# Performance work log

Hardware: AMD Instinct MI355X
Metric: run time of the kernel (lower is better)

## Reference

```python
import jax, jax.numpy as jnp
import numpy as np

B, M, N, I, O, NM = 32, 128, 128, 64, 64, 16


def setup_inputs() -> dict:
    key = jax.random.key(0)
    ks = jax.random.split(key, 10)
    def p(k, shape, s=0.02):
        return jax.random.normal(k, shape, jnp.float32) * s
    g = 1.0 / (I * O)  # xavier_normal_ gain=1/(in*out) -> tiny weights
    return {
        "x": jax.random.normal(ks[0], (B, M, N, I), jnp.float32),
        "w_spec0": p(ks[1], (2, I, O, NM, 2), g),
        "w_spec1": p(ks[2], (2, I, O, NM, 2), g),
        "w_lin": p(ks[3], (I, O)), "b_lin": jnp.zeros((O,), jnp.float32),
        "w_b1": p(ks[4], (O, 2 * O)), "b_b1": jnp.zeros((2 * O,), jnp.float32),
        "w_b2": p(ks[5], (2 * O, O)), "b_b2": jnp.zeros((O,), jnp.float32),
        "w_f1": p(ks[6], (O, 2 * O)), "b_f1": jnp.zeros((2 * O,), jnp.float32),
        "w_f2": p(ks[7], (2 * O, O)), "b_f2": jnp.zeros((O,), jnp.float32),
    }


def _complex_matmul_2d(a, w):
    # a: complex [B, I, x, y]; w: real [2, I, O, NM, 2] (factorized x-weight, y-weight)
    w0 = w[0][..., 0] + 1j * w[0][..., 1]  # [I, O, NM] complex, applied along x
    w1 = w[1][..., 0] + 1j * w[1][..., 1]  # [I, O, NM] complex, applied along y
    c = jnp.einsum('iox,bixy->boxy', w0, a)
    return jnp.einsum('bixy,ioy->boxy', c, w1)


def reference(x, w_spec0, w_spec1, w_lin, b_lin, w_b1, b_b1, w_b2, b_b2,
              w_f1, b_f1, w_f2, b_f2):
    Bv, Mv, Nv, Iv = x.shape
    nm = w_spec0.shape[3]
    Ov = w_spec0.shape[2]
    # residual branch (conv_norm=False -> Identity norm)
    res = x @ w_lin + b_lin  # [B, M, N, O]
    # spectral branch
    xt = jnp.transpose(x, (0, 3, 1, 2))  # [B, I, M, N]
    x_ft = jnp.fft.rfft2(xt, s=(Mv, Nv), norm='ortho')  # [B, I, M, N//2+1] complex64
    out_ft = jnp.zeros((Bv, Ov, Nv, Mv // 2 + 1), dtype=x_ft.dtype)  # M==N in this config
    out_ft = out_ft.at[:, :, :nm, :nm].set(_complex_matmul_2d(x_ft[:, :, :nm, :nm], w_spec0))
    out_ft = out_ft.at[:, :, -nm:, :nm].set(_complex_matmul_2d(x_ft[:, :, -nm:, :nm], w_spec1))
    y = jnp.fft.irfft2(out_ft, s=(Nv, Mv), norm='ortho')  # [B, O, N, M]
    y = jnp.transpose(y, (0, 2, 3, 1))  # [B, M, N, O]
    y = jax.nn.relu(y + res)
    bcast = jax.nn.relu(y @ w_b1 + b_b1) @ w_b2 + b_b2
    fcast = jax.nn.relu(y @ w_f1 + b_f1) @ w_f2 + b_f2
    return (bcast, fcast)
```

## Files before the change

kernel.cpp:

```cpp
#include <hip/hip_runtime.h>
#include <hip/hip_bf16.h>

#define TWO_PI 6.28318530717958647692f

typedef __attribute__((ext_vector_type(8))) short bf16x8;
typedef __attribute__((ext_vector_type(4))) float f32x4;

__device__ __forceinline__ unsigned short f2bf(float v) {
    __hip_bfloat16 h = __float2bfloat16(v);
    return *(unsigned short*)&h;
}

__device__ __forceinline__ bf16x8 cvt8(float4 a, float4 b) {
    bf16x8 r;
    r[0] = (short)f2bf(a.x); r[1] = (short)f2bf(a.y);
    r[2] = (short)f2bf(a.z); r[3] = (short)f2bf(a.w);
    r[4] = (short)f2bf(b.x); r[5] = (short)f2bf(b.y);
    r[6] = (short)f2bf(b.z); r[7] = (short)f2bf(b.w);
    return r;
}


__global__ __launch_bounds__(256) void k0_prep(const float* __restrict__ ws0,
                                               const float* __restrict__ ws1,
                                               float2* __restrict__ w0t,
                                               float2* __restrict__ w1t)
{
    int tgt = blockIdx.x * 256 + threadIdx.x;
    if (tgt < 131072) {
        int p = tgt >> 12;
        int rem = tgt & 4095;
        int i = rem >> 6, j = rem & 63;
        const float* s = (p < 16) ? ws0 : ws1;
        int px = p & 15;
        int base = ((i * 64 + j) * 16 + px) * 2;
        w0t[tgt] = make_float2(s[base], s[base + 1]);
    } else {
        int u = tgt - 131072;
        int h = u >> 16;
        int kv = (u >> 12) & 15;
        int j = (u >> 6) & 63;
        int o = u & 63;
        const float* s = (h ? ws1 : ws0) + 131072;
        int base = ((j * 64 + o) * 16 + kv) * 2;
        w1t[u] = make_float2(s[base], s[base + 1]);
    }
}

__global__ __launch_bounds__(256) void k0b_prep(const float* __restrict__ wb1,
                                                const float* __restrict__ wf1,
                                                const float* __restrict__ wb2,
                                                const float* __restrict__ wf2,
                                                const float* __restrict__ wl,
                                                unsigned short* __restrict__ w1bt,
                                                unsigned short* __restrict__ w2bt,
                                                unsigned short* __restrict__ wlt_pre,
                                                unsigned short* __restrict__ ctb_pre,
                                                unsigned short* __restrict__ wdft,
                                                unsigned short* __restrict__ e2k2,
                                                unsigned short* __restrict__ e2k4)
{
    int tgt = blockIdx.x * 256 + threadIdx.x;
    if (tgt < 16384) {
        int head = tgt >> 13;
        int o = (tgt >> 6) & 127;
        int i = tgt & 63;
        const float* src = head ? wf1 : wb1;
        int dst = head * 8192 + o * 64 + (((i >> 3) ^ (o & 7)) << 3) + (i & 7);
        w1bt[dst] = f2bf(src[i * 128 + o]);
    } else if (tgt < 32768) {
        int u = tgt - 16384;
        int head = u >> 13;
        int o = (u >> 7) & 63;
        int c = u & 127;
        const float* src = head ? wf2 : wb2;
        int dst = head * 8192 + o * 128 + (((c >> 3) ^ (o & 7)) << 3) + (c & 7);
        w2bt[dst] = f2bf(src[c * 64 + o]);
    } else if (tgt < 36864) {
        int u = tgt - 32768;
        int o = u >> 6, i = u & 63;
        int chunk = (i >> 3) ^ (o & 7);
        wlt_pre[o * 64 + chunk * 8 + (i & 7)] = f2bf(wl[i * 64 + o]);
    } else if (tgt < 40960) {
        int u = tgt - 36864;
        int v = u >> 5, k = u & 31;
        float val;
        if (k < 16) {
            val = (k == 0) ? (1.0f / 128.0f)
                           : (2.0f / 128.0f) * cosf(TWO_PI * k * v * (1.0f / 128.0f));
        } else {
            int q = k - 16;
            val = (q == 0) ? 0.f
                           : -(2.0f / 128.0f) * sinf(TWO_PI * q * v * (1.0f / 128.0f));
        }
        int chunk = (k >> 3) ^ ((v >> 1) & 3);
        ctb_pre[v * 32 + chunk * 8 + (k & 7)] = f2bf(val);
    } else if (tgt < 45312) {
        int u = tgt - 40960;
        int c = u / 2176;
        int rem = u - c * 2176;
        int kv = rem / 136, n = rem - (rem / 136) * 136;
        float val = 0.f;
        if (n < 128) {
            int idx = (kv * n) & 127;
            float th = (float)idx * (TWO_PI / 128.0f);
            val = c ? -sinf(th) : cosf(th);
        }
        wdft[u] = f2bf(val);
    } else if (tgt < 61696) {
        int u = tgt - 45312;
        int plane = u >> 13;
        int rem = u & 8191;
        int p = rem >> 8;
        int k = rem & 255;
        int km = (p < 16) ? p : (96 + p);
        int m = (k < 128) ? k : (k - 128);
        float th = (float)((km * m) & 127) * (TWO_PI / 128.0f);
        float c = cosf(th), s = sinf(th);
        float val = plane ? ((k < 128) ? -s : c) : ((k < 128) ? c : s);
        val *= (1.0f / 128.0f);
        int ch = k >> 3;
        int dst = plane * 8192 + p * 256 + (((ch & 24) | ((ch ^ p) & 7)) << 3) + (k & 7);
        e2k2[dst] = f2bf(val);
    } else {
        int u = tgt - 61696;
        int plane = u >> 13;
        int rem = u & 8191;
        int uu = rem >> 6;
        int k = rem & 63;
        int p = (k < 32) ? k : (k - 32);
        int km = (p < 16) ? p : (96 + p);
        float th = (float)((km * uu) & 127) * (TWO_PI / 128.0f);
        float c = cosf(th), s = sinf(th);
        float val = plane ? ((k < 32) ? s : c) : ((k < 32) ? c : -s);
        int ch = k >> 3;
        int dst = plane * 8192 + uu * 64 + (((ch ^ (uu & 7)) & 7) << 3) + (k & 7);
        e2k4[dst] = f2bf(val);
    }
}

__global__ __launch_bounds__(256) void k1_dft_n(const float* __restrict__ x,
                                                const unsigned short* __restrict__ wdft,
                                                unsigned int* __restrict__ A)
{
    __shared__ __align__(16) unsigned short Xt[64 * 136];
    __shared__ __align__(16) unsigned short Wl[2 * 16 * 136];
    const int t = threadIdx.x;
    const int bm = blockIdx.x;
    {
        const uint4* wg = (const uint4*)wdft;
        uint4* wl = (uint4*)Wl;
        for (int k = t; k < 544; k += 256) wl[k] = wg[k];
    }
    {
        const float* xg = x + (size_t)bm * 8192;
        const int i = t & 63, q = t >> 6;
        #pragma unroll
        for (int pass = 0; pass < 8; ++pass) {
            int n0 = pass * 16 + q * 4;
            float v0 = xg[(n0 + 0) * 64 + i];
            float v1 = xg[(n0 + 1) * 64 + i];
            float v2 = xg[(n0 + 2) * 64 + i];
            float v3 = xg[(n0 + 3) * 64 + i];
            unsigned lo = (unsigned)f2bf(v0) | ((unsigned)f2bf(v1) << 16);
            unsigned hi = (unsigned)f2bf(v2) | ((unsigned)f2bf(v3) << 16);
            *(uint2*)&Xt[i * 136 + n0] = make_uint2(lo, hi);
        }
    }
    __syncthreads();
    const int lane = t & 63, wv = t >> 6;
    const int ar = lane & 15, kg = lane >> 4;
    f32x4 are = (f32x4){0.f, 0.f, 0.f, 0.f};
    f32x4 aim = (f32x4){0.f, 0.f, 0.f, 0.f};
    #pragma unroll
    for (int ks = 0; ks < 4; ++ks) {
        int off = ks * 32 + kg * 8;
        bf16x8 b   = *(const bf16x8*)&Xt[(wv * 16 + ar) * 136 + off];
        bf16x8 wre = *(const bf16x8*)&Wl[ar * 136 + off];
        bf16x8 wim = *(const bf16x8*)&Wl[(16 + ar) * 136 + off];
        are = __builtin_amdgcn_mfma_f32_16x16x32_bf16(wre, b, are, 0, 0, 0);
        aim = __builtin_amdgcn_mfma_f32_16x16x32_bf16(wim, b, aim, 0, 0, 0);
    }
    unsigned int* Ap = A + (size_t)bm * 1024;
    #pragma unroll
    for (int r = 0; r < 4; ++r) {
        int kv = kg * 4 + r;
        int i = wv * 16 + ar;
        Ap[kv * 64 + i] = (unsigned)f2bf(are[r]) | ((unsigned)f2bf(aim[r]) << 16);
    }
}

__global__ __launch_bounds__(256) void k2_dft_m(const unsigned int* __restrict__ A,
                                                const unsigned short* __restrict__ e2k2,
                                                float2* __restrict__ xft)
{
    __shared__ __align__(16) unsigned short El[16384];
    __shared__ __align__(16) unsigned short Sl[16384];
    const int t = threadIdx.x;
    const int b = blockIdx.x >> 4, kv = blockIdx.x & 15;
    {
        const uint4* eg = (const uint4*)e2k2;
        for (int k = t; k < 2048; k += 256) ((uint4*)El)[k] = eg[k];
    }
    for (int idx = t; idx < 4096; idx += 256) {
        int m2 = idx >> 6, i = idx & 63;
        int m = m2 << 1;
        unsigned a0 = A[((size_t)(b * 128 + m) * 16 + kv) * 64 + i];
        unsigned a1 = A[((size_t)(b * 128 + m + 1) * 16 + kv) * 64 + i];
        unsigned arp = (a0 & 0xffffu) | (a1 << 16);
        unsigned aip = (a0 >> 16) | (a1 & 0xffff0000u);
        int chr = m >> 3;
        *(unsigned*)&Sl[i * 256 + (((chr & 24) | ((chr ^ i) & 7)) << 3) + (m & 7)] = arp;
        int kk = 128 + m;
        int chi = kk >> 3;
        *(unsigned*)&Sl[i * 256 + (((chi & 24) | ((chi ^ i) & 7)) << 3) + (kk & 7)] = aip;
    }
    __syncthreads();
    const int lane = t & 63, wv = t >> 6;
    const int ar = lane & 15, kg = lane >> 4;
    const int pt = wv >> 1;
    const int it0 = (wv & 1) << 1;
    #pragma unroll
    for (int iti = 0; iti < 2; ++iti) {
        int it = it0 + iti;
        int prow = pt * 16 + ar;
        int irow = it * 16 + ar;
        f32x4 accre = (f32x4){0.f, 0.f, 0.f, 0.f};
        f32x4 accim = (f32x4){0.f, 0.f, 0.f, 0.f};
        #pragma unroll
        for (int ks = 0; ks < 8; ++ks) {
            int ch = ks * 4 + kg;
            int aoff = prow * 256 + (((ch & 24) | ((ch ^ prow) & 7)) << 3);
            int boff = irow * 256 + (((ch & 24) | ((ch ^ irow) & 7)) << 3);
            bf16x8 bfrag = *(const bf16x8*)&Sl[boff];
            bf16x8 fre = *(const bf16x8*)&El[aoff];
            bf16x8 fim = *(const bf16x8*)&El[8192 + aoff];
            accre = __builtin_amdgcn_mfma_f32_16x16x32_bf16(fre, bfrag, accre, 0, 0, 0);
            accim = __builtin_amdgcn_mfma_f32_16x16x32_bf16(fim, bfrag, accim, 0, 0, 0);
        }
        #pragma unroll
        for (int r = 0; r < 4; ++r) {
            int p = pt * 16 + kg * 4 + r;
            int i = it * 16 + ar;
            xft[((size_t)(b * 32 + p) * 16 + kv) * 64 + i] =
                make_float2(accre[r], accim[r]);
        }
    }
}

__global__ __launch_bounds__(256) void k3a_spec1(const float2* __restrict__ xft,
                                                 const float2* __restrict__ w0t,
                                                 float2* __restrict__ c1)
{
    __shared__ __align__(16) float2 xs[16][64];
    __shared__ __align__(16) float2 w0s[64][64];
    const int t = threadIdx.x;
    const int b = blockIdx.x >> 5, p = blockIdx.x & 31;
    const float2* xg = xft + (size_t)(b * 32 + p) * 1024;
    for (int k = t; k < 1024; k += 256) ((float2*)xs)[k] = xg[k];
    const float4* wg = (const float4*)(w0t + (size_t)p * 4096);
    for (int k = t; k < 2048; k += 256) ((float4*)w0s)[k] = wg[k];
    __syncthreads();
    const int j = t & 63;
    const int kv0 = (t >> 6) << 2;
    float2 acc[4];
    #pragma unroll
    for (int q = 0; q < 4; ++q) acc[q] = make_float2(0.f, 0.f);
    for (int i = 0; i < 64; ++i) {
        float2 w = w0s[i][j];
        #pragma unroll
        for (int q = 0; q < 4; ++q) {
            float2 a = xs[kv0 + q][i];
            acc[q].x += a.x * w.x - a.y * w.y;
            acc[q].y += a.x * w.y + a.y * w.x;
        }
    }
    #pragma unroll
    for (int q = 0; q < 4; ++q)
        c1[((size_t)(b * 32 + p) * 16 + kv0 + q) * 64 + j] = acc[q];
}

__global__ __launch_bounds__(256) void k3b_spec2(const float2* __restrict__ c1,
                                                 const float2* __restrict__ w1t,
                                                 float2* __restrict__ oft)
{
    __shared__ __align__(16) float2 cs[16][64];
    __shared__ __align__(16) float2 w1s[64][64];
    const int t = threadIdx.x;
    int id = blockIdx.x;
    const int h = id & 1; id >>= 1;
    const int kv = id & 15; const int b = id >> 4;
    for (int k = t; k < 1024; k += 256) {
        int pp = k >> 6, j = k & 63;
        cs[pp][j] = c1[((size_t)(b * 32 + h * 16 + pp) * 16 + kv) * 64 + j];
    }
    const float4* wg = (const float4*)(w1t + (size_t)(h * 16 + kv) * 4096);
    for (int k = t; k < 2048; k += 256) ((float4*)w1s)[k] = wg[k];
    __syncthreads();
    const int o = t & 63;
    const int pp0 = (t >> 6) << 2;
    float2 acc[4];
    #pragma unroll
    for (int q = 0; q < 4; ++q) acc[q] = make_float2(0.f, 0.f);
    for (int j = 0; j < 64; ++j) {
        float2 w = w1s[j][o];
        #pragma unroll
        for (int q = 0; q < 4; ++q) {
            float2 a = cs[pp0 + q][j];
            acc[q].x += a.x * w.x - a.y * w.y;
            acc[q].y += a.x * w.y + a.y * w.x;
        }
    }
    #pragma unroll
    for (int q = 0; q < 4; ++q)
        oft[((size_t)(b * 32 + h * 16 + pp0 + q) * 16 + kv) * 64 + o] = acc[q];
}

__global__ __launch_bounds__(256) void k4_idft_m(const float2* __restrict__ oft,
                                                 const unsigned short* __restrict__ e2k4,
                                                 unsigned int* __restrict__ T)
{
    __shared__ __align__(16) unsigned short El[16384];
    __shared__ __align__(16) unsigned short Sl[4096];
    const int t = threadIdx.x;
    const int b = blockIdx.x >> 4, q = blockIdx.x & 15;
    {
        const uint4* eg = (const uint4*)e2k4;
        for (int k = t; k < 2048; k += 256) ((uint4*)El)[k] = eg[k];
    }
    for (int idx = t; idx < 1024; idx += 256) {
        int p2 = idx >> 6, o = idx & 63;
        int p = p2 << 1;
        float2 v0 = oft[((size_t)(b * 32 + p) * 16 + q) * 64 + o];
        float2 v1 = oft[((size_t)(b * 32 + p + 1) * 16 + q) * 64 + o];
        unsigned rep = (unsigned)f2bf(v0.x) | ((unsigned)f2bf(v1.x) << 16);
        unsigned imp = (unsigned)f2bf(v0.y) | ((unsigned)f2bf(v1.y) << 16);
        int chr = p >> 3;
        *(unsigned*)&Sl[o * 64 + ((chr ^ (o & 7)) << 3) + (p & 7)] = rep;
        int kk = 32 + p;
        int chi = kk >> 3;
        *(unsigned*)&Sl[o * 64 + ((chi ^ (o & 7)) << 3) + (kk & 7)] = imp;
    }
    __syncthreads();
    const int lane = t & 63, wv = t >> 6;
    const int ar = lane & 15, kg = lane >> 4;
    unsigned int* Tp = T + ((size_t)b * 128) * 1024 + (size_t)q * 64;
    #pragma unroll
    for (int uti = 0; uti < 2; ++uti) {
        int ut = wv * 2 + uti;
        int urow = ut * 16 + ar;
        int aswz = urow & 7;
        #pragma unroll
        for (int ot = 0; ot < 4; ++ot) {
            int orow = ot * 16 + ar;
            f32x4 accre = (f32x4){0.f, 0.f, 0.f, 0.f};
            f32x4 accim = (f32x4){0.f, 0.f, 0.f, 0.f};
            #pragma unroll
            for (int ks = 0; ks < 2; ++ks) {
                int ch = ks * 4 + kg;
                int aoff = urow * 64 + ((ch ^ aswz) << 3);
                int boff = orow * 64 + ((ch ^ (orow & 7)) << 3);
                bf16x8 bfrag = *(const bf16x8*)&Sl[boff];
                bf16x8 fre = *(const bf16x8*)&El[aoff];
                bf16x8 fim = *(const bf16x8*)&El[8192 + aoff];
                accre = __builtin_amdgcn_mfma_f32_16x16x32_bf16(fre, bfrag, accre, 0, 0, 0);
                accim = __builtin_amdgcn_mfma_f32_16x16x32_bf16(fim, bfrag, accim, 0, 0, 0);
            }
            #pragma unroll
            for (int r = 0; r < 4; ++r) {
                int u = ut * 16 + kg * 4 + r;
                int o = ot * 16 + ar;
                Tp[(size_t)u * 1024 + o] =
                    (unsigned)f2bf(accre[r]) | ((unsigned)f2bf(accim[r]) << 16);
            }
        }
    }
}

__global__ __launch_bounds__(256) void k56_fused(
    const float* __restrict__ x, const unsigned int* __restrict__ Tg,
    const float* __restrict__ bl,
    const unsigned short* __restrict__ ctb_pre, const unsigned short* __restrict__ wlt_pre,
    const unsigned short* __restrict__ w1bt, const unsigned short* __restrict__ w2bt,
    const float* __restrict__ bb1, const float* __restrict__ bb2,
    const float* __restrict__ bf1, const float* __restrict__ bf2,
    float* __restrict__ out)
{
    __shared__ __align__(16) unsigned char U[32768];
    __shared__ __align__(16) unsigned short ys[2][8192];
    __shared__ __align__(16) unsigned short hs[8192];

    unsigned short* Ctb = (unsigned short*)U;
    unsigned short* wlt = (unsigned short*)(U + 8192);
    unsigned short* Tpk = (unsigned short*)(U + 16384);
    unsigned short* w1s = (unsigned short*)U;
    unsigned short* w2s = (unsigned short*)(U + 16384);

    const int t = threadIdx.x;
    const int bm0 = blockIdx.x << 1;
    const int lane = t & 63, wv = t >> 6;
    const int ar = lane & 15, kg = lane >> 4;
    const int R0 = wv * 32;

    float4 xr[2][2][4];
    #pragma unroll
    for (int g = 0; g < 2; ++g)
        #pragma unroll
        for (int rt = 0; rt < 2; ++rt) {
            const float* xp = x + (size_t)(bm0 + g) * 8192 + (R0 + rt * 16 + ar) * 64 + kg * 8;
            xr[g][rt][0] = *(const float4*)(xp);
            xr[g][rt][1] = *(const float4*)(xp + 4);
            xr[g][rt][2] = *(const float4*)(xp + 32);
            xr[g][rt][3] = *(const float4*)(xp + 36);
        }

    {
        const uint4* cg = (const uint4*)ctb_pre;
        for (int k = t; k < 512; k += 256) ((uint4*)Ctb)[k] = cg[k];
        const uint4* wg = (const uint4*)wlt_pre;
        for (int k = t; k < 512; k += 256) ((uint4*)wlt)[k] = wg[k];
        for (int idx = t; idx < 2048; idx += 256) {
            int g = idx >> 10, rem = idx & 1023;
            int q = rem >> 6, o = rem & 63;
            unsigned v = Tg[(size_t)(bm0 + g) * 1024 + rem];
            int f = (o >> 1) & 3;
            unsigned short* Tp = Tpk + g * 2048;
            Tp[o * 32 + (((q >> 3) ^ f) << 3) + (q & 7)] = (unsigned short)(v & 0xffffu);
            Tp[o * 32 + (((2 + (q >> 3)) ^ f) << 3) + (q & 7)] = (unsigned short)(v >> 16);
        }
    }
    __syncthreads();

    float biasl[4];
    #pragma unroll
    for (int ct = 0; ct < 4; ++ct) biasl[ct] = bl[ct * 16 + ar];

    #pragma unroll
    for (int g = 0; g < 2; ++g) {
        const unsigned short* Tp = Tpk + g * 2048;
        #pragma unroll
        for (int rt = 0; rt < 2; ++rt) {
            const int vrow = R0 + rt * 16 + ar;
            bf16x8 a0 = cvt8(xr[g][rt][0], xr[g][rt][1]);
            bf16x8 a1 = cvt8(xr[g][rt][2], xr[g][rt][3]);
            bf16x8 asp = *(const bf16x8*)&Ctb[vrow * 32 + ((kg ^ ((vrow >> 1) & 3)) << 3)];
            f32x4 acc[4];
            #pragma unroll
            for (int ct = 0; ct < 4; ++ct) acc[ct] = (f32x4){0.f, 0.f, 0.f, 0.f};
            #pragma unroll
            for (int ct = 0; ct < 4; ++ct) {
                int o = ct * 16 + ar;
                bf16x8 b0 = *(const bf16x8*)&wlt[o * 64 + ((kg ^ (o & 7)) << 3)];
                bf16x8 b1 = *(const bf16x8*)&wlt[o * 64 + (((4 + kg) ^ (o & 7)) << 3)];
                bf16x8 bsp = *(const bf16x8*)&Tp[o * 32 + ((kg ^ ((o >> 1) & 3)) << 3)];
                acc[ct] = __builtin_amdgcn_mfma_f32_16x16x32_bf16(a0, b0, acc[ct], 0, 0, 0);
                acc[ct] = __builtin_amdgcn_mfma_f32_16x16x32_bf16(a1, b1, acc[ct], 0, 0, 0);
                acc[ct] = __builtin_amdgcn_mfma_f32_16x16x32_bf16(asp, bsp, acc[ct], 0, 0, 0);
            }
            #pragma unroll
            for (int ct = 0; ct < 4; ++ct) {
                int col = ct * 16 + ar;
                #pragma unroll
                for (int r = 0; r < 4; ++r) {
                    int row = R0 + rt * 16 + kg * 4 + r;
                    float v = fmaxf(acc[ct][r] + biasl[ct], 0.f);
                    ys[g][row * 64 + (((col >> 3) ^ (row & 7)) << 3) + (col & 7)] = f2bf(v);
                }
            }
        }
    }
    __syncthreads();

    unsigned short* hw = hs + wv * 2048;
    for (int head = 0; head < 2; ++head) {
        {
            const uint4* g1 = (const uint4*)(w1bt + head * 8192);
            for (int k = t; k < 1024; k += 256) ((uint4*)w1s)[k] = g1[k];
            const uint4* g2 = (const uint4*)(w2bt + head * 8192);
            for (int k = t; k < 1024; k += 256) ((uint4*)w2s)[k] = g2[k];
        }
        const float* B1 = head ? bf1 : bb1;
        const float* B2 = head ? bf2 : bb2;
        float bias1[8], bias2[4];
        #pragma unroll
        for (int c = 0; c < 8; ++c) bias1[c] = B1[c * 16 + ar];
        #pragma unroll
        for (int c = 0; c < 4; ++c) bias2[c] = B2[c * 16 + ar];
        __syncthreads();

        #pragma unroll
        for (int g = 0; g < 2; ++g) {
            #pragma unroll
            for (int rt = 0; rt < 2; ++rt) {
                const int rowbase = R0 + rt * 16;
                const int yrow = rowbase + ar;
                bf16x8 ya0 = *(const bf16x8*)&ys[g][yrow * 64 + ((kg ^ (yrow & 7)) << 3)];
                bf16x8 ya1 = *(const bf16x8*)&ys[g][yrow * 64 + (((4 + kg) ^ (yrow & 7)) << 3)];
                f32x4 acc1[8];
                #pragma unroll
                for (int ct = 0; ct < 8; ++ct) acc1[ct] = (f32x4){0.f, 0.f, 0.f, 0.f};
                #pragma unroll
                for (int ct = 0; ct < 8; ++ct) {
                    int brow = ct * 16 + ar;
                    bf16x8 b0 = *(const bf16x8*)&w1s[brow * 64 + ((kg ^ (brow & 7)) << 3)];
                    bf16x8 b1 = *(const bf16x8*)&w1s[brow * 64 + (((4 + kg) ^ (brow & 7)) << 3)];
                    acc1[ct] = __builtin_amdgcn_mfma_f32_16x16x32_bf16(ya0, b0, acc1[ct], 0, 0, 0);
                    acc1[ct] = __builtin_amdgcn_mfma_f32_16x16x32_bf16(ya1, b1, acc1[ct], 0, 0, 0);
                }
                #pragma unroll
                for (int ct = 0; ct < 8; ++ct) {
                    #pragma unroll
                    for (int r = 0; r < 4; ++r) {
                        int row = kg * 4 + r;
                        int col = ct * 16 + ar;
                        float v = fmaxf(acc1[ct][r] + bias1[ct], 0.f);
                        hw[row * 128 + (((col >> 3) ^ (row & 7)) << 3) + (col & 7)] = f2bf(v);
                    }
                }
                f32x4 acc2[4];
                #pragma unroll
                for (int ct = 0; ct < 4; ++ct) acc2[ct] = (f32x4){0.f, 0.f, 0.f, 0.f};
                #pragma unroll
                for (int ks = 0; ks < 4; ++ks) {
                    bf16x8 a = *(const bf16x8*)&hw[ar * 128 + (((ks * 4 + kg) ^ (ar & 7)) << 3)];
                    #pragma unroll
                    for (int ct = 0; ct < 4; ++ct) {
                        int brow = ct * 16 + ar;
                        bf16x8 b = *(const bf16x8*)&w2s[brow * 128 + (((ks * 4 + kg) ^ (ar & 7)) << 3)];
                        acc2[ct] = __builtin_amdgcn_mfma_f32_16x16x32_bf16(a, b, acc2[ct], 0, 0, 0);
                    }
                }
                float* og = out + (size_t)head * 33554432u + (size_t)(bm0 + g) * 8192;
                #pragma unroll
                for (int ct = 0; ct < 4; ++ct) {
                    #pragma unroll
                    for (int r = 0; r < 4; ++r)
                        og[(size_t)(rowbase + kg * 4 + r) * 64 + ct * 16 + ar] =
                            acc2[ct][r] + bias2[ct];
                }
            }
        }
        if (head == 0) __syncthreads();
    }
}

extern "C" void kernel_launch(void* const* d_in, const int* in_sizes, int n_in,
                              void* d_out, int out_size, void* d_ws, size_t ws_size,
                              hipStream_t stream)
{
    (void)in_sizes; (void)n_in; (void)out_size; (void)ws_size;
    const float* x   = (const float*)d_in[0];
    const float* ws0 = (const float*)d_in[1];
    const float* ws1 = (const float*)d_in[2];
    const float* wl  = (const float*)d_in[3];
    const float* bl  = (const float*)d_in[4];
    const float* wb1 = (const float*)d_in[5];
    const float* bb1 = (const float*)d_in[6];
    const float* wb2 = (const float*)d_in[7];
    const float* bb2 = (const float*)d_in[8];
    const float* wf1 = (const float*)d_in[9];
    const float* bf1 = (const float*)d_in[10];
    const float* wf2 = (const float*)d_in[11];
    const float* bf2 = (const float*)d_in[12];
    float* out = (float*)d_out;

    float* ws = (float*)d_ws;
    float2* w0t = (float2*)ws;
    float2* w1t = (float2*)(ws + 262144);
    unsigned int* Tb  = (unsigned int*)(ws + 524288);
    unsigned int* Ab  = (unsigned int*)(ws + 8912896);
    float2* xft = (float2*)(ws + 17301504);
    float2* c1b = (float2*)(ws + 19398656);
    float2* oft = (float2*)(ws + 21495808);
    unsigned short* w1bt    = (unsigned short*)(ws + 23592960);
    unsigned short* w2bt    = (unsigned short*)(ws + 23601152);
    unsigned short* wlt_pre = (unsigned short*)(ws + 23609344);
    unsigned short* ctb_pre = (unsigned short*)(ws + 23611392);
    unsigned short* wdft    = (unsigned short*)(ws + 23613440);
    unsigned short* e2k2    = (unsigned short*)(ws + 23615616);
    unsigned short* e2k4    = (unsigned short*)(ws + 23623808);

    k0_prep    <<<1024, 256, 0, stream>>>(ws0, ws1, w0t, w1t);
    k0b_prep   <<<305,  256, 0, stream>>>(wb1, wf1, wb2, wf2, wl,
                                          w1bt, w2bt, wlt_pre, ctb_pre, wdft,
                                          e2k2, e2k4);
    k1_dft_n   <<<4096, 256, 0, stream>>>(x, wdft, Ab);
    k2_dft_m   <<<512,  256, 0, stream>>>(Ab, e2k2, xft);
    k3a_spec1  <<<1024, 256, 0, stream>>>(xft, w0t, c1b);
    k3b_spec2  <<<1024, 256, 0, stream>>>(c1b, w1t, oft);
    k4_idft_m  <<<512,  256, 0, stream>>>(oft, e2k4, Tb);
    k56_fused  <<<2048, 256, 0, stream>>>(x, Tb, bl, ctb_pre, wlt_pre,
                                          w1bt, w2bt, bb1, bb2, bf1, bf2, out);
}
```

Before: 218.2 us.

## Run spectral mode-mixing matmuls on bf16 MFMA with packed bf16 intermediates

Replaces the scalar fp32 complex multiply-accumulate loops in the two spectral weight kernels with bf16 MFMA instructions. Weights are pre-laid-out as real-block complex matrices ([re,-im; im,re]) in swizzled bf16 tiles. The intermediates between the DFT, spectral and inverse-DFT stages are stored as packed bf16 re/im pairs instead of float2, halving that memory traffic. This trades precision for throughput, and the weight prep kernel now launches more threads to write the expanded layout.

```diff
diff --git a/kernel.cpp b/kernel.cpp
--- a/kernel.cpp
+++ b/kernel.cpp
@@ -20,31 +20,36 @@
     return r;
 }
 
+#define SWZ128(row, ch) ((((ch) & 8) | (((ch) ^ ((row) & 7)) & 7)) << 3)
+
 
 __global__ __launch_bounds__(256) void k0_prep(const float* __restrict__ ws0,
                                                const float* __restrict__ ws1,
-                                               float2* __restrict__ w0t,
-                                               float2* __restrict__ w1t)
+                                               unsigned short* __restrict__ w0cc,
+                                               unsigned short* __restrict__ w1cc)
 {
     int tgt = blockIdx.x * 256 + threadIdx.x;
-    if (tgt < 131072) {
-        int p = tgt >> 12;
-        int rem = tgt & 4095;
-        int i = rem >> 6, j = rem & 63;
-        const float* s = (p < 16) ? ws0 : ws1;
-        int px = p & 15;
-        int base = ((i * 64 + j) * 16 + px) * 2;
-        w0t[tgt] = make_float2(s[base], s[base + 1]);
+    int which = tgt >> 19;
+    int u = tgt & 524287;
+    int ps = u >> 14;
+    int plane = (u >> 13) & 1;
+    int row = (u >> 7) & 63;
+    int k = u & 127;
+    int half = k >> 6, e = k & 63;
+    float re, im;
+    if (which == 0) {
+        const float* s = (ps < 16) ? ws0 : ws1;
+        int base = ((e * 64 + row) * 16 + (ps & 15)) * 2;
+        re = s[base]; im = s[base + 1];
     } else {
-        int u = tgt - 131072;
-        int h = u >> 16;
-        int kv = (u >> 12) & 15;
-        int j = (u >> 6) & 63;
-        int o = u & 63;
-        const float* s = (h ? ws1 : ws0) + 131072;
-        int base = ((j * 64 + o) * 16 + kv) * 2;
-        w1t[u] = make_float2(s[base], s[base + 1]);
-    }
+        const float* s = ((ps >> 4) ? ws1 : ws0) + 131072;
+        int base = ((e * 64 + row) * 16 + (ps & 15)) * 2;
+        re = s[base]; im = s[base + 1];
+    }
+    float val = plane ? (half ? re : im) : (half ? -im : re);
+    int ch = k >> 3;
+    int dst = ps * 16384 + plane * 8192 + row * 128 + SWZ128(row, ch) + (k & 7);
+    (which ? w1cc : w0cc)[dst] = f2bf(val);
 }
 
 __global__ __launch_bounds__(256) void k0b_prep(const float* __restrict__ wb1,
@@ -192,7 +197,7 @@
 
 __global__ __launch_bounds__(256) void k2_dft_m(const unsigned int* __restrict__ A,
                                                 const unsigned short* __restrict__ e2k2,
-                                                float2* __restrict__ xft)
+                                                unsigned int* __restrict__ xftp)
 {
     __shared__ __align__(16) unsigned short El[16384];
     __shared__ __align__(16) unsigned short Sl[16384];
@@ -242,81 +247,110 @@
         for (int r = 0; r < 4; ++r) {
             int p = pt * 16 + kg * 4 + r;
             int i = it * 16 + ar;
-            xft[((size_t)(b * 32 + p) * 16 + kv) * 64 + i] =
-                make_float2(accre[r], accim[r]);
-        }
-    }
-}
-
-__global__ __launch_bounds__(256) void k3a_spec1(const float2* __restrict__ xft,
-                                                 const float2* __restrict__ w0t,
-                                                 float2* __restrict__ c1)
-{
-    __shared__ __align__(16) float2 xs[16][64];
-    __shared__ __align__(16) float2 w0s[64][64];
+            xftp[((size_t)(b * 32 + p) * 16 + kv) * 64 + i] =
+                (unsigned)f2bf(accre[r]) | ((unsigned)f2bf(accim[r]) << 16);
+        }
+    }
+}
+
+__global__ __launch_bounds__(256) void k3a_spec1(const unsigned int* __restrict__ xftp,
+                                                 const unsigned short* __restrict__ w0cc,
+                                                 unsigned int* __restrict__ c1p)
+{
+    __shared__ __align__(16) unsigned short As[16 * 128];
+    __shared__ __align__(16) unsigned short Ws[2 * 64 * 128];
     const int t = threadIdx.x;
     const int b = blockIdx.x >> 5, p = blockIdx.x & 31;
-    const float2* xg = xft + (size_t)(b * 32 + p) * 1024;
-    for (int k = t; k < 1024; k += 256) ((float2*)xs)[k] = xg[k];
-    const float4* wg = (const float4*)(w0t + (size_t)p * 4096);
-    for (int k = t; k < 2048; k += 256) ((float4*)w0s)[k] = wg[k];
+    {
+        const uint4* wg = (const uint4*)(w0cc + (size_t)p * 16384);
+        for (int k = t; k < 2048; k += 256) ((uint4*)Ws)[k] = wg[k];
+    }
+    for (int idx = t; idx < 512; idx += 256) {
+        int kvv = idx >> 5, i2 = (idx & 31) << 1;
+        const unsigned* src = xftp + ((size_t)(b * 32 + p) * 16 + kvv) * 64;
+        unsigned a0 = src[i2], a1 = src[i2 + 1];
+        unsigned rep = (a0 & 0xffffu) | (a1 << 16);
+        unsigned imp = (a0 >> 16) | (a1 & 0xffff0000u);
+        int chr = i2 >> 3;
+        *(unsigned*)&As[kvv * 128 + SWZ128(kvv, chr) + (i2 & 7)] = rep;
+        int kk = 64 + i2;
+        int chi = kk >> 3;
+        *(unsigned*)&As[kvv * 128 + SWZ128(kvv, chi) + (kk & 7)] = imp;
+    }
     __syncthreads();
-    const int j = t & 63;
-    const int kv0 = (t >> 6) << 2;
-    float2 acc[4];
-    #pragma unroll
-    for (int q = 0; q < 4; ++q) acc[q] = make_float2(0.f, 0.f);
-    for (int i = 0; i < 64; ++i) {
-        float2 w = w0s[i][j];
-        #pragma unroll
-        for (int q = 0; q < 4; ++q) {
-            float2 a = xs[kv0 + q][i];
-            acc[q].x += a.x * w.x - a.y * w.y;
-            acc[q].y += a.x * w.y + a.y * w.x;
-        }
-    }
-    #pragma unroll
-    for (int q = 0; q < 4; ++q)
-        c1[((size_t)(b * 32 + p) * 16 + kv0 + q) * 64 + j] = acc[q];
-}
-
-__global__ __launch_bounds__(256) void k3b_spec2(const float2* __restrict__ c1,
-                                                 const float2* __restrict__ w1t,
-                                                 float2* __restrict__ oft)
-{
-    __shared__ __align__(16) float2 cs[16][64];
-    __shared__ __align__(16) float2 w1s[64][64];
+    const int lane = t & 63, wv = t >> 6;
+    const int ar = lane & 15, kg = lane >> 4;
+    const int jrow = wv * 16 + ar;
+    f32x4 accre = (f32x4){0.f, 0.f, 0.f, 0.f};
+    f32x4 accim = (f32x4){0.f, 0.f, 0.f, 0.f};
+    #pragma unroll
+    for (int ks = 0; ks < 4; ++ks) {
+        int ch = ks * 4 + kg;
+        bf16x8 af = *(const bf16x8*)&As[ar * 128 + SWZ128(ar, ch)];
+        bf16x8 br = *(const bf16x8*)&Ws[jrow * 128 + SWZ128(jrow, ch)];
+        bf16x8 bi = *(const bf16x8*)&Ws[8192 + jrow * 128 + SWZ128(jrow, ch)];
+        accre = __builtin_amdgcn_mfma_f32_16x16x32_bf16(af, br, accre, 0, 0, 0);
+        accim = __builtin_amdgcn_mfma_f32_16x16x32_bf16(af, bi, accim, 0, 0, 0);
+    }
+    unsigned int* cp = c1p + ((size_t)(b * 32 + p) * 16) * 64;
+    #pragma unroll
+    for (int r = 0; r < 4; ++r) {
+        int kv = kg * 4 + r;
+        cp[kv * 64 + wv * 16 + ar] =
+            (unsigned)f2bf(accre[r]) | ((unsigned)f2bf(accim[r]) << 16);
+    }
+}
+
+__global__ __launch_bounds__(256) void k3b_spec2(const unsigned int* __restrict__ c1p,
+                                                 const unsigned short* __restrict__ w1cc,
+                                                 unsigned int* __restrict__ oftp)
+{
+    __shared__ __align__(16) unsigned short As[16 * 128];
+    __shared__ __align__(16) unsigned short Ws[2 * 64 * 128];
     const int t = threadIdx.x;
     int id = blockIdx.x;
     const int h = id & 1; id >>= 1;
     const int kv = id & 15; const int b = id >> 4;
-    for (int k = t; k < 1024; k += 256) {
-        int pp = k >> 6, j = k & 63;
-        cs[pp][j] = c1[((size_t)(b * 32 + h * 16 + pp) * 16 + kv) * 64 + j];
-    }
-    const float4* wg = (const float4*)(w1t + (size_t)(h * 16 + kv) * 4096);
-    for (int k = t; k < 2048; k += 256) ((float4*)w1s)[k] = wg[k];
+    {
+        const uint4* wg = (const uint4*)(w1cc + (size_t)(h * 16 + kv) * 16384);
+        for (int k = t; k < 2048; k += 256) ((uint4*)Ws)[k] = wg[k];
+    }
+    for (int idx = t; idx < 512; idx += 256) {
+        int pp = idx >> 5, j2 = (idx & 31) << 1;
+        const unsigned* src = c1p + ((size_t)(b * 32 + h * 16 + pp) * 16 + kv) * 64;
+        unsigned a0 = src[j2], a1 = src[j2 + 1];
+        unsigned rep = (a0 & 0xffffu) | (a1 << 16);
+        unsigned imp = (a0 >> 16) | (a1 & 0xffff0000u);
+        int chr = j2 >> 3;
+        *(unsigned*)&As[pp * 128 + SWZ128(pp, chr) + (j2 & 7)] = rep;
+        int kk = 64 + j2;
+        int chi = kk >> 3;
+        *(unsigned*)&As[pp * 128 + SWZ128(pp, chi) + (kk & 7)] = imp;
+    }
     __syncthreads();
-    const int o = t & 63;
-    const int pp0 = (t >> 6) << 2;
-    float2 acc[4];
-    #pragma unroll
-    for (int q = 0; q < 4; ++q) acc[q] = make_float2(0.f, 0.f);
-    for (int j = 0; j < 64; ++j) {
-        float2 w = w1s[j][o];
-        #pragma unroll
-        for (int q = 0; q < 4; ++q) {
-            float2 a = cs[pp0 + q][j];
-            acc[q].x += a.x * w.x - a.y * w.y;
-            acc[q].y += a.x * w.y + a.y * w.x;
-        }
-    }
-    #pragma unroll
-    for (int q = 0; q < 4; ++q)
-        oft[((size_t)(b * 32 + h * 16 + pp0 + q) * 16 + kv) * 64 + o] = acc[q];
-}
-
-__global__ __launch_bounds__(256) void k4_idft_m(const float2* __restrict__ oft,
+    const int lane = t & 63, wv = t >> 6;
+    const int ar = lane & 15, kg = lane >> 4;
+    const int orow = wv * 16 + ar;
+    f32x4 accre = (f32x4){0.f, 0.f, 0.f, 0.f};
+    f32x4 accim = (f32x4){0.f, 0.f, 0.f, 0.f};
+    #pragma unroll
+    for (int ks = 0; ks < 4; ++ks) {
+        int ch = ks * 4 + kg;
+        bf16x8 af = *(const bf16x8*)&As[ar * 128 + SWZ128(ar, ch)];
+        bf16x8 br = *(const bf16x8*)&Ws[orow * 128 + SWZ128(orow, ch)];
+        bf16x8 bi = *(const bf16x8*)&Ws[8192 + orow * 128 + SWZ128(orow, ch)];
+        accre = __builtin_amdgcn_mfma_f32_16x16x32_bf16(af, br, accre, 0, 0, 0);
+        accim = __builtin_amdgcn_mfma_f32_16x16x32_bf16(af, bi, accim, 0, 0, 0);
+    }
+    #pragma unroll
+    for (int r = 0; r < 4; ++r) {
+        int pp = kg * 4 + r;
+        oftp[((size_t)(b * 32 + h * 16 + pp) * 16 + kv) * 64 + orow] =
+            (unsigned)f2bf(accre[r]) | ((unsigned)f2bf(accim[r]) << 16);
+    }
+}
+
+__global__ __launch_bounds__(256) void k4_idft_m(const unsigned int* __restrict__ oftp,
                                                  const unsigned short* __restrict__ e2k4,
                                                  unsigned int* __restrict__ T)
 {
@@ -331,10 +365,10 @@
     for (int idx = t; idx < 1024; idx += 256) {
         int p2 = idx >> 6, o = idx & 63;
         int p = p2 << 1;
-        float2 v0 = oft[((size_t)(b * 32 + p) * 16 + q) * 64 + o];
-        float2 v1 = oft[((size_t)(b * 32 + p + 1) * 16 + q) * 64 + o];
-        unsigned rep = (unsigned)f2bf(v0.x) | ((unsigned)f2bf(v1.x) << 16);
-        unsigned imp = (unsigned)f2bf(v0.y) | ((unsigned)f2bf(v1.y) << 16);
+        unsigned a0 = oftp[((size_t)(b * 32 + p) * 16 + q) * 64 + o];
+        unsigned a1 = oftp[((size_t)(b * 32 + p + 1) * 16 + q) * 64 + o];
+        unsigned rep = (a0 & 0xffffu) | (a1 << 16);
+        unsigned imp = (a0 >> 16) | (a1 & 0xffff0000u);
         int chr = p >> 3;
         *(unsigned*)&Sl[o * 64 + ((chr ^ (o & 7)) << 3) + (p & 7)] = rep;
         int kk = 32 + p;
@@ -565,13 +599,13 @@
     float* out = (float*)d_out;
 
     float* ws = (float*)d_ws;
-    float2* w0t = (float2*)ws;
-    float2* w1t = (float2*)(ws + 262144);
-    unsigned int* Tb  = (unsigned int*)(ws + 524288);
-    unsigned int* Ab  = (unsigned int*)(ws + 8912896);
-    float2* xft = (float2*)(ws + 17301504);
-    float2* c1b = (float2*)(ws + 19398656);
-    float2* oft = (float2*)(ws + 21495808);
+    unsigned short* w0cc = (unsigned short*)ws;
+    unsigned short* w1cc = (unsigned short*)(ws + 262144);
+    unsigned int* Tb   = (unsigned int*)(ws + 524288);
+    unsigned int* Ab   = (unsigned int*)(ws + 8912896);
+    unsigned int* xftp = (unsigned int*)(ws + 17301504);
+    unsigned int* c1p  = (unsigned int*)(ws + 19398656);
+    unsigned int* oftp = (unsigned int*)(ws + 21495808);
     unsigned short* w1bt    = (unsigned short*)(ws + 23592960);
     unsigned short* w2bt    = (unsigned short*)(ws + 23601152);
     unsigned short* wlt_pre = (unsigned short*)(ws + 23609344);
@@ -580,15 +614,15 @@
     unsigned short* e2k2    = (unsigned short*)(ws + 23615616);
     unsigned short* e2k4    = (unsigned short*)(ws + 23623808);
 
-    k0_prep    <<<1024, 256, 0, stream>>>(ws0, ws1, w0t, w1t);
+    k0_prep    <<<4096, 256, 0, stream>>>(ws0, ws1, w0cc, w1cc);
     k0b_prep   <<<305,  256, 0, stream>>>(wb1, wf1, wb2, wf2, wl,
                                           w1bt, w2bt, wlt_pre, ctb_pre, wdft,
                                           e2k2, e2k4);
     k1_dft_n   <<<4096, 256, 0, stream>>>(x, wdft, Ab);
-    k2_dft_m   <<<512,  256, 0, stream>>>(Ab, e2k2, xft);
-    k3a_spec1  <<<1024, 256, 0, stream>>>(xft, w0t, c1b);
-    k3b_spec2  <<<1024, 256, 0, stream>>>(c1b, w1t, oft);
-    k4_idft_m  <<<512,  256, 0, stream>>>(oft, e2k4, Tb);
+    k2_dft_m   <<<512,  256, 0, stream>>>(Ab, e2k2, xftp);
+    k3a_spec1  <<<1024, 256, 0, stream>>>(xftp, w0cc, c1p);
+    k3b_spec2  <<<1024, 256, 0, stream>>>(c1p, w1cc, oftp);
+    k4_idft_m  <<<512,  256, 0, stream>>>(oftp, e2k4, Tb);
     k56_fused  <<<2048, 256, 0, stream>>>(x, Tb, bl, ctb_pre, wlt_pre,
                                           w1bt, w2bt, bb1, bb2, bf1, bf2, out);
 }
```

Measured after the change: 192.2 us (median of 3 runs). 11.9% less time.
